# Optimization experiments

Measured on AMD Instinct MI355X. Metric: run time of the kernel, lower is better.

## Reference

```python
import jax, jax.numpy as jnp
import numpy as np

WD, WH, WW = 4, 8, 8
N_WIN = WD * WH * WW  # 256 tokens per window
NUM_HEADS = 8
DIM = 512
HIDDEN = int(DIM * 4.0)
SHIFT = (2, 4, 4)
EPS = 1e-5


def _rel_pos_index():
    coords = np.stack(np.meshgrid(np.arange(WD), np.arange(WH), np.arange(WW), indexing='ij'))
    cf = coords.reshape(3, -1)  # [3, N]
    rc = cf[:, :, None] - cf[:, None, :]  # [3, N, N]
    rc = rc.transpose(1, 2, 0).astype(np.int64)
    rc[:, :, 0] += WD - 1
    rc[:, :, 1] += WH - 1
    rc[:, :, 2] += WW - 1
    rc[:, :, 0] *= (2 * WH - 1) * (2 * WW - 1)
    rc[:, :, 1] *= (2 * WW - 1)
    return jnp.asarray(rc.sum(-1))  # [N, N]

REL_IDX = _rel_pos_index()


def setup_inputs() -> dict:
    key = jax.random.key(0)
    ks = jax.random.split(key, 10)
    B, D, H, W = 1, 16, 64, 64
    L = D * H * W
    s = 0.02
    table_size = (2 * WD - 1) * (2 * WH - 1) * (2 * WW - 1)  # 1575
    return {
        'x': jax.random.normal(ks[0], (B, L, DIM), jnp.float32),
        't_emb': jax.random.normal(ks[1], (B, DIM), jnp.float32),
        'ada_w': jax.random.normal(ks[2], (DIM, 6 * DIM), jnp.float32) * s,
        'ada_b': jnp.zeros((6 * DIM,), jnp.float32),
        'rel_table': jax.random.normal(ks[3], (table_size, NUM_HEADS), jnp.float32) * s,
        'qkv_w': jax.random.normal(ks[4], (DIM, 3 * DIM), jnp.float32) * s,
        'qkv_b': jnp.zeros((3 * DIM,), jnp.float32),
        'proj_w': jax.random.normal(ks[5], (DIM, DIM), jnp.float32) * s,
        'proj_b': jnp.zeros((DIM,), jnp.float32),
        'fc1_w': jax.random.normal(ks[6], (DIM, HIDDEN), jnp.float32) * s,
        'fc1_b': jnp.zeros((HIDDEN,), jnp.float32),
        'fc2_w': jax.random.normal(ks[7], (HIDDEN, DIM), jnp.float32) * s,
        'fc2_b': jnp.zeros((DIM,), jnp.float32),
        'D': D, 'H': H, 'W': W,
    }


def _layernorm(y):
    m = jnp.mean(y, axis=-1, keepdims=True)
    v = jnp.mean(jnp.square(y - m), axis=-1, keepdims=True)
    return (y - m) * jax.lax.rsqrt(v + EPS)


def _window_partition(x3, D, H, W):
    B, _, _, _, C = x3.shape
    x3 = x3.reshape(B, D // WD, WD, H // WH, WH, W // WW, WW, C)
    x3 = x3.transpose(0, 1, 3, 5, 2, 4, 6, 7)
    return x3.reshape(-1, N_WIN, C)


def _window_reverse(win, B, D, H, W):
    C = win.shape[-1]
    x3 = win.reshape(B, D // WD, H // WH, W // WW, WD, WH, WW, C)
    x3 = x3.transpose(0, 1, 4, 2, 5, 3, 6, 7)
    return x3.reshape(B, D, H, W, C)


def _window_attention(xn, rel_table, qkv_w, qkv_b, proj_w, proj_b):
    Bn, N, C = xn.shape
    h, d = NUM_HEADS, C // NUM_HEADS
    qkv = (xn @ qkv_w + qkv_b).reshape(Bn, N, 3, h, d).transpose(2, 0, 3, 1, 4)
    q, k, v = qkv[0], qkv[1], qkv[2]
    scale = d ** -0.5
    attn = jnp.einsum('bhnd,bhmd->bhnm', q * scale, k)  # [Bn, h, N, N]
    bias = rel_table[REL_IDX]  # gather -> [N, N, h]
    attn = jax.nn.softmax(attn + bias.transpose(2, 0, 1)[None], axis=-1)
    o = jnp.einsum('bhnm,bhmd->bhnd', attn, v)
    o = o.transpose(0, 2, 1, 3).reshape(Bn, N, C)
    return o @ proj_w + proj_b


def reference(x, t_emb, ada_w, ada_b, rel_table, qkv_w, qkv_b, proj_w, proj_b,
              fc1_w, fc1_b, fc2_w, fc2_b, D, H, W):
    B, L, C = x.shape
    mod = jax.nn.silu(t_emb) @ ada_w + ada_b  # [B, 6C]
    shift_msa, scale_msa, gate_msa, shift_mlp, scale_mlp, gate_mlp = jnp.split(mod, 6, axis=-1)

    x3 = x.reshape(B, D, H, W, C)
    x3 = jnp.roll(x3, shift=(-SHIFT[0], -SHIFT[1], -SHIFT[2]), axis=(1, 2, 3))
    xw = _window_partition(x3, D, H, W)  # [B*nW, N, C]

    xn = _layernorm(xw) * (1.0 + scale_msa[:, None, :]) + shift_msa[:, None, :]
    attn_out = _window_attention(xn, rel_table, qkv_w, qkv_b, proj_w, proj_b)
    xw = xw + gate_msa[:, None, :] * attn_out

    x3 = _window_reverse(xw, B, D, H, W)
    x3 = jnp.roll(x3, shift=SHIFT, axis=(1, 2, 3))
    x = x3.reshape(B, L, C)

    xn = _layernorm(x) * (1.0 + scale_mlp[:, None, :]) + shift_mlp[:, None, :]
    h1 = jax.nn.gelu(xn @ fc1_w + fc1_b, approximate=False)
    mlp_out = h1 @ fc2_w + fc2_b
    return x + gate_mlp[:, None, :] * mlp_out
```

## Files before the change

kernel.cpp:

```cpp
#include <hip/hip_runtime.h>
#include <hip/hip_bf16.h>
#include <math.h>


typedef __attribute__((ext_vector_type(8))) short short8;
typedef __attribute__((ext_vector_type(4))) short bs4;
typedef __attribute__((ext_vector_type(4))) float f32x4;

typedef const __attribute__((address_space(1))) unsigned int gu32;
typedef __attribute__((address_space(3))) unsigned int lu32;

__device__ __forceinline__ float bf2f(short s) {
  unsigned int u = ((unsigned int)(unsigned short)s) << 16;
  float f;
  __builtin_memcpy(&f, &u, 4);
  return f;
}
__device__ __forceinline__ short f2bf(float f) {
  unsigned int u;
  __builtin_memcpy(&u, &f, 4);
  u += 0x7FFFu + ((u >> 16) & 1u);
  return (short)(u >> 16);
}
__device__ __forceinline__ short f2bf_trunc(float f) {
  unsigned int u;
  __builtin_memcpy(&u, &f, 4);
  return (short)(u >> 16);
}

__device__ __forceinline__ int win_to_src(int p) {
  int wi = p >> 8, t = p & 255;
  int sd = (((wi >> 6) << 2) + (t >> 6) + 2) & 15;
  int sh = ((((wi >> 3) & 7) << 3) + ((t >> 3) & 7) + 4) & 63;
  int sw = (((wi & 7) << 3) + (t & 7) + 4) & 63;
  return (sd << 12) | (sh << 6) | sw;
}

__global__ __launch_bounds__(256) void mod_kernel(
    const float* __restrict__ t_emb, const float* __restrict__ ada_w,
    const float* __restrict__ ada_b, float* __restrict__ mod) {
  __shared__ float sl[512];
  int tid = threadIdx.x;
  for (int r = 0; r < 2; ++r) {
    float x = t_emb[r * 256 + tid];
    sl[r * 256 + tid] = x / (1.f + expf(-x));
  }
  __syncthreads();
  int col = blockIdx.x * 256 + tid;
  float acc = ada_b[col];
  for (int k = 0; k < 512; ++k)
    acc += sl[k] * ada_w[(size_t)k * 3072 + col];
  mod[col] = acc;
}

__global__ __launch_bounds__(256) void bias_kernel(
    const float* __restrict__ rel_table, short* __restrict__ biasT) {
  int head = blockIdx.x >> 8;
  int j = blockIdx.x & 255;
  int i = threadIdx.x;
  int di = i >> 6, hi = (i >> 3) & 7, wi = i & 7;
  int dj = j >> 6, hj = (j >> 3) & 7, wj = j & 7;
  int idx = (di - dj + 3) * 225 + (hi - hj + 7) * 15 + (wi - wj + 7);
  biasT[(size_t)blockIdx.x * 256 + i] = f2bf(rel_table[idx * 8 + head]);
}

__global__ __launch_bounds__(256) void transpose_kernel(
    const float* __restrict__ in, short* __restrict__ out, int K, int N) {
  __shared__ short t[32][33];
  int n0 = blockIdx.x * 32, k0 = blockIdx.y * 32;
  int tx = threadIdx.x & 31, ty = threadIdx.x >> 5;
#pragma unroll
  for (int r = 0; r < 4; ++r)
    t[ty + r * 8][tx] = f2bf(in[(size_t)(k0 + ty + r * 8) * N + n0 + tx]);
  __syncthreads();
#pragma unroll
  for (int r = 0; r < 4; ++r)
    out[(size_t)(n0 + ty + r * 8) * K + k0 + tx] = t[tx][ty + r * 8];
}

template <int GATHER>
__global__ __launch_bounds__(256) void ln_kernel(
    const float* __restrict__ xin, short* __restrict__ xout,
    const float* __restrict__ shv, const float* __restrict__ scv) {
  int wave = threadIdx.x >> 6, lane = threadIdx.x & 63;
  int p = blockIdx.x * 4 + wave;
  int s = GATHER ? win_to_src(p) : p;
  const f32x4* px = (const f32x4*)(xin + (size_t)s * 512 + lane * 8);
  f32x4 a = px[0], b = px[1];
  float xs[8];
#pragma unroll
  for (int j = 0; j < 4; ++j) { xs[j] = a[j]; xs[4 + j] = b[j]; }
  float sum = 0.f, sq = 0.f;
#pragma unroll
  for (int j = 0; j < 8; ++j) { sum += xs[j]; sq += xs[j] * xs[j]; }
#pragma unroll
  for (int off = 1; off < 64; off <<= 1) {
    sum += __shfl_xor(sum, off, 64);
    sq += __shfl_xor(sq, off, 64);
  }
  float mean = sum * (1.f / 512.f);
  float var = sq * (1.f / 512.f) - mean * mean;
  float rs = rsqrtf(var + 1e-5f);
  short8 o;
#pragma unroll
  for (int j = 0; j < 8; ++j) {
    int c = lane * 8 + j;
    float val = (xs[j] - mean) * rs * (1.f + scv[c]) + shv[c];
    o[j] = f2bf(val);
  }
  *(short8*)(xout + (size_t)p * 512 + lane * 8) = o;
}

template <int EPI>
__global__ __launch_bounds__(256) void gemm_kernel(
    const short* __restrict__ A, const short* __restrict__ BT,
    const float* __restrict__ bias, void* __restrict__ Cv,
    int M, int N, int K, int nbn,
    const float* __restrict__ resid, const float* __restrict__ gate) {
  __shared__ __align__(16) short Atl[128 * 64];
  __shared__ __align__(16) short Btl[128 * 64];

  int nwg = gridDim.x;
  int bid = blockIdx.x;
  int q = nwg >> 3, r = nwg & 7;
  int xcd = bid & 7, idx = bid >> 3;
  int swz = (xcd < r ? xcd * (q + 1) : r * (q + 1) + (xcd - r) * q) + idx;
  int bm = swz / nbn, bn = swz % nbn;

  int tid = threadIdx.x;
  int lane = tid & 63, wave = tid >> 6;
  int l15 = lane & 15, lg = lane >> 4;
  int wr = (wave >> 1) * 64, wc = (wave & 1) * 64;

  const size_t rowb = (size_t)K * 2;
  const char* ga[4];
  const char* gb[4];
  char* la[4];
  char* lb[4];
#pragma unroll
  for (int rr = 0; rr < 4; ++rr) {
    int o = rr * 4096 + tid * 16;
    int so = o ^ (((o >> 7) & 7) << 4);
    int row = so >> 7, cb = so & 127;
    la[rr] = (char*)Atl + o;
    lb[rr] = (char*)Btl + o;
    ga[rr] = (const char*)A + (size_t)(bm * 128 + row) * rowb + cb;
    gb[rr] = (const char*)BT + (size_t)(bn * 128 + row) * rowb + cb;
  }

  f32x4 acc[4][4];
#pragma unroll
  for (int m = 0; m < 4; ++m)
#pragma unroll
    for (int n = 0; n < 4; ++n) acc[m][n] = (f32x4){0.f, 0.f, 0.f, 0.f};

  for (int kt = 0; kt < K; kt += 64) {
#pragma unroll
    for (int rr = 0; rr < 4; ++rr) {
      __builtin_amdgcn_global_load_lds((gu32*)ga[rr], (lu32*)la[rr], 16, 0, 0);
      __builtin_amdgcn_global_load_lds((gu32*)gb[rr], (lu32*)lb[rr], 16, 0, 0);
      ga[rr] += 128;
      gb[rr] += 128;
    }
    __syncthreads();

    short8 af[2][4], bfr[2][4];
    int swr = (l15 & 7) << 4;
#pragma unroll
    for (int m = 0; m < 4; ++m) {
      int base = (wr + m * 16 + l15) * 128;
#pragma unroll
      for (int ks = 0; ks < 2; ++ks)
        af[ks][m] = *(const short8*)((const char*)Atl + base + ((ks * 64 + lg * 16) ^ swr));
    }
#pragma unroll
    for (int n = 0; n < 4; ++n) {
      int base = (wc + n * 16 + l15) * 128;
#pragma unroll
      for (int ks = 0; ks < 2; ++ks)
        bfr[ks][n] = *(const short8*)((const char*)Btl + base + ((ks * 64 + lg * 16) ^ swr));
    }
#pragma unroll
    for (int ks = 0; ks < 2; ++ks)
#pragma unroll
      for (int m = 0; m < 4; ++m)
#pragma unroll
        for (int n = 0; n < 4; ++n)
          acc[m][n] = __builtin_amdgcn_mfma_f32_16x16x32_bf16(af[ks][m], bfr[ks][n], acc[m][n], 0, 0, 0);
    __syncthreads();
  }

#pragma unroll
  for (int m = 0; m < 4; ++m)
#pragma unroll
    for (int n = 0; n < 4; ++n) {
      int col = bn * 128 + wc + n * 16 + l15;
      float bv = bias[col];
#pragma unroll
      for (int i = 0; i < 4; ++i) {
        int row = bm * 128 + wr + m * 16 + lg * 4 + i;
        float v = acc[m][n][i] + bv;
        if (EPI == 0) {
          ((short*)Cv)[(size_t)row * N + col] = f2bf(v);
        } else if (EPI == 1) {
          v = 0.5f * v * (1.f + erff(v * 0.70710678118f));
          ((short*)Cv)[(size_t)row * N + col] = f2bf(v);
        } else if (EPI == 2) {
          int s = win_to_src(row);
          float xv = resid[(size_t)s * 512 + col];
          ((float*)Cv)[(size_t)s * 512 + col] = xv + gate[col] * v;
        } else {
          float xv = resid[(size_t)row * 512 + col];
          ((float*)Cv)[(size_t)row * 512 + col] = xv + gate[col] * v;
        }
      }
    }
}

__global__ __launch_bounds__(256) void attn_kernel(
    const short* __restrict__ qkv, const short* __restrict__ biasT,
    short* __restrict__ aout) {
  __shared__ __align__(16) short vt[64][264];
  __shared__ __align__(16) short pl[4][64][40];
  int win = blockIdx.x, head = blockIdx.y;
  int tid = threadIdx.x, lane = tid & 63, wave = tid >> 6;
  int l15 = lane & 15, lg = lane >> 4;
  const short* qp = qkv + (size_t)win * 256 * 1536 + head * 64;
  const short* kp = qp + 512;
  const short* vp = qp + 1024;

#pragma unroll
  for (int r = 0; r < 8; ++r) {
    short8 vv = *(const short8*)(vp + (size_t)tid * 1536 + r * 8);
#pragma unroll
    for (int j = 0; j < 8; ++j) vt[r * 8 + j][tid] = vv[j];
  }

  short8 qf[4][2];
#pragma unroll
  for (int m = 0; m < 4; ++m)
#pragma unroll
    for (int kk = 0; kk < 2; ++kk)
      qf[m][kk] = *(const short8*)(qp + (size_t)(wave * 64 + m * 16 + l15) * 1536 + kk * 32 + lg * 8);

  __syncthreads();

  float mrun[4][4], lrun[4][4];
  f32x4 ao[4][4];
#pragma unroll
  for (int m = 0; m < 4; ++m)
#pragma unroll
    for (int i = 0; i < 4; ++i) { mrun[m][i] = -1e30f; lrun[m][i] = 0.f; }
#pragma unroll
  for (int m = 0; m < 4; ++m)
#pragma unroll
    for (int n = 0; n < 4; ++n) ao[m][n] = (f32x4){0.f, 0.f, 0.f, 0.f};

  for (int kc = 0; kc < 4; ++kc) {
    f32x4 sv[4][4];
#pragma unroll
    for (int m = 0; m < 4; ++m)
#pragma unroll
      for (int n = 0; n < 4; ++n) sv[m][n] = (f32x4){0.f, 0.f, 0.f, 0.f};
#pragma unroll
    for (int n = 0; n < 4; ++n)
#pragma unroll
      for (int kk = 0; kk < 2; ++kk) {
        short8 kf = *(const short8*)(kp + (size_t)(kc * 64 + n * 16 + l15) * 1536 + kk * 32 + lg * 8);
#pragma unroll
        for (int m = 0; m < 4; ++m)
          sv[m][n] = __builtin_amdgcn_mfma_f32_16x16x32_bf16(qf[m][kk], kf, sv[m][n], 0, 0, 0);
      }
#pragma unroll
    for (int n = 0; n < 4; ++n) {
      const short* bq = biasT + (size_t)(head * 256 + kc * 64 + n * 16 + l15) * 256 + wave * 64 + lg * 4;
#pragma unroll
      for (int m = 0; m < 4; ++m) {
        bs4 bt = *(const bs4*)(bq + m * 16);
#pragma unroll
        for (int i = 0; i < 4; ++i)
          sv[m][n][i] = sv[m][n][i] * 0.125f + bf2f(bt[i]);
      }
    }
#pragma unroll
    for (int m = 0; m < 4; ++m)
#pragma unroll
      for (int i = 0; i < 4; ++i) {
        float mx = fmaxf(fmaxf(sv[m][0][i], sv[m][1][i]), fmaxf(sv[m][2][i], sv[m][3][i]));
#pragma unroll
        for (int off = 1; off < 16; off <<= 1) mx = fmaxf(mx, __shfl_xor(mx, off, 64));
        float nm = fmaxf(mrun[m][i], mx);
        float corr = __expf(mrun[m][i] - nm);
        mrun[m][i] = nm;
        float rs = 0.f;
#pragma unroll
        for (int n = 0; n < 4; ++n) {
          float pe = __expf(sv[m][n][i] - nm);
          sv[m][n][i] = pe;
          rs += pe;
        }
#pragma unroll
        for (int off = 1; off < 16; off <<= 1) rs += __shfl_xor(rs, off, 64);
        lrun[m][i] = lrun[m][i] * corr + rs;
#pragma unroll
        for (int n = 0; n < 4; ++n) ao[m][n][i] *= corr;
      }
#pragma unroll
    for (int s = 0; s < 2; ++s) {
#pragma unroll
      for (int m = 0; m < 4; ++m)
#pragma unroll
        for (int nn = 0; nn < 2; ++nn) {
          int n = 2 * s + nn;
#pragma unroll
          for (int i = 0; i < 4; ++i)
            pl[wave][m * 16 + lg * 4 + i][nn * 16 + l15] = f2bf_trunc(sv[m][n][i]);
        }
      short8 pf[4];
#pragma unroll
      for (int m = 0; m < 4; ++m)
        pf[m] = *(const short8*)&pl[wave][m * 16 + l15][lg * 8];
#pragma unroll
      for (int n2 = 0; n2 < 4; ++n2) {
        short8 vf = *(const short8*)&vt[n2 * 16 + l15][kc * 64 + s * 32 + lg * 8];
#pragma unroll
        for (int m = 0; m < 4; ++m)
          ao[m][n2] = __builtin_amdgcn_mfma_f32_16x16x32_bf16(pf[m], vf, ao[m][n2], 0, 0, 0);
      }
    }
  }

#pragma unroll
  for (int m = 0; m < 4; ++m)
#pragma unroll
    for (int i = 0; i < 4; ++i) {
      float inv = 1.f / lrun[m][i];
      int row = win * 256 + wave * 64 + m * 16 + lg * 4 + i;
#pragma unroll
      for (int n = 0; n < 4; ++n)
        aout[(size_t)row * 512 + head * 64 + n * 16 + l15] = f2bf(ao[m][n][i] * inv);
    }
}

extern "C" void kernel_launch(void* const* d_in, const int* in_sizes, int n_in,
                              void* d_out, int out_size, void* d_ws, size_t ws_size,
                              hipStream_t stream) {
  (void)in_sizes; (void)n_in; (void)out_size; (void)ws_size;
  const float* x         = (const float*)d_in[0];
  const float* t_emb     = (const float*)d_in[1];
  const float* ada_w     = (const float*)d_in[2];
  const float* ada_b     = (const float*)d_in[3];
  const float* rel_table = (const float*)d_in[4];
  const float* qkv_w     = (const float*)d_in[5];
  const float* qkv_b     = (const float*)d_in[6];
  const float* proj_w    = (const float*)d_in[7];
  const float* proj_b    = (const float*)d_in[8];
  const float* fc1_w     = (const float*)d_in[9];
  const float* fc1_b     = (const float*)d_in[10];
  const float* fc2_w     = (const float*)d_in[11];
  const float* fc2_b     = (const float*)d_in[12];
  float* out = (float*)d_out;
  char* ws = (char*)d_ws;

  float* mod    = (float*)(ws);
  short* biasT  = (short*)(ws + 16384);
  short* qkvwT  = (short*)(ws + 16384 + 2097152);
  short* projwT = qkvwT + 1536 * 512;
  short* fc1wT  = projwT + 512 * 512;
  short* fc2wT  = fc1wT + 2048 * 512;
  short* xn     = (short*)(ws + 8404992);
  short* qkvb   = xn + (size_t)65536 * 512;
  short* attno  = qkvb + (size_t)65536 * 1536;
  short* h1     = qkvb;
  float* x2     = out;

  mod_kernel<<<12, 256, 0, stream>>>(t_emb, ada_w, ada_b, mod);
  bias_kernel<<<2048, 256, 0, stream>>>(rel_table, biasT);
  transpose_kernel<<<dim3(48, 16), 256, 0, stream>>>(qkv_w, qkvwT, 512, 1536);
  transpose_kernel<<<dim3(16, 16), 256, 0, stream>>>(proj_w, projwT, 512, 512);
  transpose_kernel<<<dim3(64, 16), 256, 0, stream>>>(fc1_w, fc1wT, 512, 2048);
  transpose_kernel<<<dim3(16, 64), 256, 0, stream>>>(fc2_w, fc2wT, 2048, 512);

  ln_kernel<1><<<16384, 256, 0, stream>>>(x, xn, mod + 0, mod + 512);
  gemm_kernel<0><<<512 * 12, 256, 0, stream>>>(xn, qkvwT, qkv_b, qkvb,
                                               65536, 1536, 512, 12, nullptr, nullptr);
  attn_kernel<<<dim3(256, 8), 256, 0, stream>>>(qkvb, biasT, attno);
  gemm_kernel<2><<<512 * 4, 256, 0, stream>>>(attno, projwT, proj_b, x2,
                                              65536, 512, 512, 4, x, mod + 1024);
  ln_kernel<0><<<16384, 256, 0, stream>>>(x2, xn, mod + 1536, mod + 2048);
  gemm_kernel<1><<<512 * 16, 256, 0, stream>>>(xn, fc1wT, fc1_b, h1,
                                               65536, 2048, 512, 16, nullptr, nullptr);
  gemm_kernel<3><<<512 * 4, 256, 0, stream>>>(h1, fc2wT, fc2_b, out,
                                              65536, 512, 2048, 4, x2, mod + 2560);
}
```

Before: 1.040 ms.

## Use 256x128 GEMM tiles with 512 threads, tanh GELU, prescaled Q

The GEMM kernel moves to 512 threads and a 256x128 output tile. The A tile in shared memory doubles and each block's B tile is reused across more rows, cutting global traffic per output. The exact erf GELU is swapped for a tanh-style sigmoid approximation, and bf16 stores now truncate instead of rounding. In attention, the 1/8 softmax scale is folded into Q at load time, which adds a bf16 truncation of the scaled Q. These changes trade numerical accuracy for fewer instructions, and the larger tile may lower occupancy.

```diff
diff --git a/kernel.cpp b/kernel.cpp
--- a/kernel.cpp
+++ b/kernel.cpp
@@ -112,12 +112,12 @@
 }
 
 template <int EPI>
-__global__ __launch_bounds__(256) void gemm_kernel(
+__global__ __launch_bounds__(512) void gemm_kernel(
     const short* __restrict__ A, const short* __restrict__ BT,
     const float* __restrict__ bias, void* __restrict__ Cv,
     int M, int N, int K, int nbn,
     const float* __restrict__ resid, const float* __restrict__ gate) {
-  __shared__ __align__(16) short Atl[128 * 64];
+  __shared__ __align__(16) short Atl[256 * 64];
   __shared__ __align__(16) short Btl[128 * 64];
 
   int nwg = gridDim.x;
@@ -134,17 +134,22 @@
 
   const size_t rowb = (size_t)K * 2;
   const char* ga[4];
-  const char* gb[4];
-  char* la[4];
-  char* lb[4];
+  const char* gb[2];
+  int loA[4], loB[2];
 #pragma unroll
   for (int rr = 0; rr < 4; ++rr) {
-    int o = rr * 4096 + tid * 16;
+    int o = rr * 8192 + tid * 16;
     int so = o ^ (((o >> 7) & 7) << 4);
     int row = so >> 7, cb = so & 127;
-    la[rr] = (char*)Atl + o;
-    lb[rr] = (char*)Btl + o;
-    ga[rr] = (const char*)A + (size_t)(bm * 128 + row) * rowb + cb;
+    loA[rr] = o;
+    ga[rr] = (const char*)A + (size_t)(bm * 256 + row) * rowb + cb;
+  }
+#pragma unroll
+  for (int rr = 0; rr < 2; ++rr) {
+    int o = rr * 8192 + tid * 16;
+    int so = o ^ (((o >> 7) & 7) << 4);
+    int row = so >> 7, cb = so & 127;
+    loB[rr] = o;
     gb[rr] = (const char*)BT + (size_t)(bn * 128 + row) * rowb + cb;
   }
 
@@ -154,18 +159,22 @@
 #pragma unroll
     for (int n = 0; n < 4; ++n) acc[m][n] = (f32x4){0.f, 0.f, 0.f, 0.f};
 
+  const int swr = (l15 & 7) << 4;
+
   for (int kt = 0; kt < K; kt += 64) {
 #pragma unroll
     for (int rr = 0; rr < 4; ++rr) {
-      __builtin_amdgcn_global_load_lds((gu32*)ga[rr], (lu32*)la[rr], 16, 0, 0);
-      __builtin_amdgcn_global_load_lds((gu32*)gb[rr], (lu32*)lb[rr], 16, 0, 0);
+      __builtin_amdgcn_global_load_lds((gu32*)ga[rr], (lu32*)((char*)Atl + loA[rr]), 16, 0, 0);
       ga[rr] += 128;
+    }
+#pragma unroll
+    for (int rr = 0; rr < 2; ++rr) {
+      __builtin_amdgcn_global_load_lds((gu32*)gb[rr], (lu32*)((char*)Btl + loB[rr]), 16, 0, 0);
       gb[rr] += 128;
     }
     __syncthreads();
 
     short8 af[2][4], bfr[2][4];
-    int swr = (l15 & 7) << 4;
 #pragma unroll
     for (int m = 0; m < 4; ++m) {
       int base = (wr + m * 16 + l15) * 128;
@@ -198,13 +207,14 @@
       float bv = bias[col];
 #pragma unroll
       for (int i = 0; i < 4; ++i) {
-        int row = bm * 128 + wr + m * 16 + lg * 4 + i;
+        int row = bm * 256 + wr + m * 16 + lg * 4 + i;
         float v = acc[m][n][i] + bv;
         if (EPI == 0) {
-          ((short*)Cv)[(size_t)row * N + col] = f2bf(v);
+          ((short*)Cv)[(size_t)row * N + col] = f2bf_trunc(v);
         } else if (EPI == 1) {
-          v = 0.5f * v * (1.f + erff(v * 0.70710678118f));
-          ((short*)Cv)[(size_t)row * N + col] = f2bf(v);
+          float tt = v * (0.7978845608f + 0.0356774081f * v * v);
+          float sg = 1.f / (1.f + __expf(-2.f * tt));
+          ((short*)Cv)[(size_t)row * N + col] = f2bf_trunc(v * sg);
         } else if (EPI == 2) {
           int s = win_to_src(row);
           float xv = resid[(size_t)s * 512 + col];
@@ -240,8 +250,12 @@
 #pragma unroll
   for (int m = 0; m < 4; ++m)
 #pragma unroll
-    for (int kk = 0; kk < 2; ++kk)
-      qf[m][kk] = *(const short8*)(qp + (size_t)(wave * 64 + m * 16 + l15) * 1536 + kk * 32 + lg * 8);
+    for (int kk = 0; kk < 2; ++kk) {
+      short8 v = *(const short8*)(qp + (size_t)(wave * 64 + m * 16 + l15) * 1536 + kk * 32 + lg * 8);
+#pragma unroll
+      for (int j = 0; j < 8; ++j) v[j] = f2bf_trunc(bf2f(v[j]) * 0.125f);
+      qf[m][kk] = v;
+    }
 
   __syncthreads();
 
@@ -279,7 +293,7 @@
         bs4 bt = *(const bs4*)(bq + m * 16);
 #pragma unroll
         for (int i = 0; i < 4; ++i)
-          sv[m][n][i] = sv[m][n][i] * 0.125f + bf2f(bt[i]);
+          sv[m][n][i] = sv[m][n][i] + bf2f(bt[i]);
       }
     }
 #pragma unroll
@@ -382,14 +396,14 @@
   transpose_kernel<<<dim3(16, 64), 256, 0, stream>>>(fc2_w, fc2wT, 2048, 512);
 
   ln_kernel<1><<<16384, 256, 0, stream>>>(x, xn, mod + 0, mod + 512);
-  gemm_kernel<0><<<512 * 12, 256, 0, stream>>>(xn, qkvwT, qkv_b, qkvb,
+  gemm_kernel<0><<<256 * 12, 512, 0, stream>>>(xn, qkvwT, qkv_b, qkvb,
                                                65536, 1536, 512, 12, nullptr, nullptr);
   attn_kernel<<<dim3(256, 8), 256, 0, stream>>>(qkvb, biasT, attno);
-  gemm_kernel<2><<<512 * 4, 256, 0, stream>>>(attno, projwT, proj_b, x2,
+  gemm_kernel<2><<<256 * 4, 512, 0, stream>>>(attno, projwT, proj_b, x2,
                                               65536, 512, 512, 4, x, mod + 1024);
   ln_kernel<0><<<16384, 256, 0, stream>>>(x2, xn, mod + 1536, mod + 2048);
-  gemm_kernel<1><<<512 * 16, 256, 0, stream>>>(xn, fc1wT, fc1_b, h1,
+  gemm_kernel<1><<<256 * 16, 512, 0, stream>>>(xn, fc1wT, fc1_b, h1,
                                                65536, 2048, 512, 16, nullptr, nullptr);
-  gemm_kernel<3><<<512 * 4, 256, 0, stream>>>(h1, fc2wT, fc2_b, out,
+  gemm_kernel<3><<<256 * 4, 512, 0, stream>>>(h1, fc2wT, fc2_b, out,
                                               65536, 512, 2048, 4, x2, mod + 2560);
 }
```

After: 898.4 us. -13.6%, faster.
